# Performance work log

Hardware: AMD Instinct MI355X
Metric: run time of the kernel (lower is better)

The kernel has to match this reference:

```python
import jax, jax.numpy as jnp
import numpy as np

T, B, D, H = 1024, 64, 256, 256


def setup_inputs() -> dict:
    key = jax.random.key(0)
    ks = jax.random.split(key, 7)
    u = lambda k, shape: jax.random.uniform(k, shape, jnp.float32, -0.1, 0.1)
    x = jax.random.normal(ks[0], (T, B, D), dtype=jnp.float32)
    # gate order along last axis: f, g, i, o (each block of width H)
    fwd_W = u(ks[1], (D, 4 * H))
    fwd_U = u(ks[2], (H, 4 * H))
    fwd_b = u(ks[3], (4 * H,))
    bwd_W = u(ks[4], (D, 4 * H))
    bwd_U = u(ks[5], (H, 4 * H))
    bwd_b = u(ks[6], (4 * H,))
    return {"x": x, "fwd_W": fwd_W, "fwd_U": fwd_U, "fwd_b": fwd_b,
            "bwd_W": bwd_W, "bwd_U": bwd_U, "bwd_b": bwd_b}


def _lstm_scan(x, W, U, b):
    # x: [T, B, D]; returns (hs [T,B,H], h_last [B,H])
    Bsz = x.shape[1]
    h0 = jnp.zeros((Bsz, H), x.dtype)
    c0 = jnp.zeros((Bsz, H), x.dtype)
    xW = x @ W  # precompute input projections: [T, B, 4H]

    def step(carry, xw_t):
        h, c = carry
        z = xw_t + h @ U + b  # [B, 4H]
        f = jax.nn.sigmoid(z[:, 0 * H:1 * H])
        g = jnp.tanh(z[:, 1 * H:2 * H])
        i = jax.nn.sigmoid(z[:, 2 * H:3 * H])
        o = jax.nn.sigmoid(z[:, 3 * H:4 * H])
        c_new = c * f + g * i
        h_new = o * jnp.tanh(c_new)
        return (h_new, c_new), h_new

    (h_last, _), hs = jax.lax.scan(step, (h0, c0), xW)
    return hs, h_last


def reference(x, fwd_W, fwd_U, fwd_b, bwd_W, bwd_U, bwd_b):
    hs_f, h_f = _lstm_scan(x, fwd_W, fwd_U, fwd_b)
    hs_b_rev, h_b = _lstm_scan(x[::-1], bwd_W, bwd_U, bwd_b)
    hs_b = hs_b_rev[::-1]
    output = jnp.concatenate([hs_f, hs_b], axis=-1)  # [T, B, 2H]
    return (output, h_f, h_b)
```

## Files before the change

### kernel.cpp

```cpp
#include <hip/hip_runtime.h>

#define T_STEPS 1024
#define BATCH   64
#define NDIM    256
#define HID     256
#define G4      1024

typedef short bf16x8 __attribute__((ext_vector_type(8)));
typedef float f32x4  __attribute__((ext_vector_type(4)));
typedef unsigned short u16;

#define XW_ELEMS ((size_t)2 * T_STEPS * BATCH * G4)
#define UT_ELEMS ((size_t)2 * 4 * 65536)
#define WT_ELEMS UT_ELEMS

__device__ __forceinline__ float b2f(u16 v) {
  union { unsigned u; float f; } c; c.u = ((unsigned)v) << 16; return c.f;
}
__device__ __forceinline__ u16 f2b(float f) {
  union { float f; unsigned u; } c; c.f = f;
  unsigned u = c.u;
  u += 0x7fffu + ((u >> 16) & 1u);
  return (u16)(u >> 16);
}
__device__ __forceinline__ float sigm(float x) {
  float e = __expf(-x);
  return __builtin_amdgcn_rcpf(1.0f + e);
}
__device__ __forceinline__ float tanh_f(float x) {
  return 2.0f * sigm(2.0f * x) - 1.0f;
}

__global__ __launch_bounds__(1024) void build_ut(
    const float* __restrict__ U0, const float* __restrict__ U1,
    u16* __restrict__ UT)
{
  const int d = blockIdx.x >> 2;
  const int g = blockIdx.x & 3;
  const float* __restrict__ U = d ? U1 : U0;
  const int w = threadIdx.x >> 6, lane = threadIdx.x & 63;
  const int q = lane >> 4, c15 = lane & 15;
  u16* dst = UT + ((size_t)d * 4 + g) * 65536;
  #pragma unroll
  for (int kf = 0; kf < 8; ++kf) {
    bf16x8 v;
    #pragma unroll
    for (int j = 0; j < 8; ++j)
      v[j] = (short)f2b(U[(size_t)(kf * 32 + q * 8 + j) * G4 + g * 256 + w * 16 + c15]);
    ((bf16x8*)dst)[((w * 8 + kf) << 6) + lane] = v;
  }
}

__global__ __launch_bounds__(256, 2) void xw_gemm_v2(
    const float* __restrict__ x,
    const u16* __restrict__ WT,
    const float* __restrict__ b0, const float* __restrict__ b1,
    u16* __restrict__ xw)
{
  const int t0   = blockIdx.x * 2;
  const int lane = threadIdx.x & 63;
  const int wv   = threadIdx.x >> 6;
  const int q    = lane >> 4;
  const int c15  = lane & 15;

  __shared__ __align__(16) u16 Alds[2 * 64 * 256];

  #pragma unroll
  for (int t01 = 0; t01 < 2; ++t01) {
    const float* xt = x + (size_t)(t0 + t01) * BATCH * NDIM;
    #pragma unroll
    for (int i = 0; i < 8; ++i) {
      int g = (int)threadIdx.x + 256 * i;
      int r = g >> 5, c = g & 31;
      const float* src = xt + r * 256 + c * 8;
      bf16x8 v;
      #pragma unroll
      for (int j = 0; j < 8; ++j) v[j] = (short)f2b(src[j]);
      int cs = (c & 16) | ((c ^ (r & 15)) & 15);
      ((bf16x8*)Alds)[t01 * 2048 + r * 32 + cs] = v;
    }
  }
  __syncthreads();

  bf16x8 af2[2][8];
  const int arow = wv * 16 + c15;
  #pragma unroll
  for (int t01 = 0; t01 < 2; ++t01) {
    #pragma unroll
    for (int kf = 0; kf < 8; ++kf) {
      int c = kf * 4 + q;
      int cs = (c & 16) | ((c ^ c15) & 15);
      af2[t01][kf] = ((const bf16x8*)Alds)[t01 * 2048 + arow * 32 + cs];
    }
  }

  for (int iter = 0; iter < 32; ++iter) {
    const int d  = iter >> 4;
    const int n0 = (iter & 15) * 64;
    const float* __restrict__ bias = d ? b1 : b0;

    bf16x8 uf[4][8];
    float bc[4];
    #pragma unroll
    for (int ct = 0; ct < 4; ++ct) {
      const int ncol = n0 + ct * 16;
      const int g2 = ncol >> 8, wcol = (ncol >> 4) & 15;
      const bf16x8* wsrc = (const bf16x8*)(WT + ((size_t)d * 4 + g2) * 65536);
      #pragma unroll
      for (int kf = 0; kf < 8; ++kf)
        uf[ct][kf] = wsrc[((wcol * 8 + kf) << 6) + lane];
      bc[ct] = bias[ncol + c15];
    }

    #pragma unroll
    for (int t01 = 0; t01 < 2; ++t01) {
      f32x4 acc[4];
      #pragma unroll
      for (int ct = 0; ct < 4; ++ct) acc[ct] = (f32x4){0.f, 0.f, 0.f, 0.f};
      #pragma unroll
      for (int kf = 0; kf < 8; ++kf) {
        #pragma unroll
        for (int ct = 0; ct < 4; ++ct)
          acc[ct] = __builtin_amdgcn_mfma_f32_16x16x32_bf16(af2[t01][kf], uf[ct][kf], acc[ct], 0, 0, 0);
      }

      u16* dst = xw + (((size_t)d * T_STEPS + (t0 + t01)) * 4 + wv) * 16384;
      #pragma unroll
      for (int ct = 0; ct < 4; ++ct) {
        int ncol = n0 + ct * 16;
        int g2 = ncol >> 8, w2 = (ncol >> 4) & 15;
        union { u16 s[4]; uint2 v; } pk;
        #pragma unroll
        for (int r = 0; r < 4; ++r) pk.s[r] = f2b(acc[ct][r] + bc[ct]);
        *(uint2*)(dst + (size_t)(w2 * 64 + q * 16 + c15) * 16 + g2 * 4) = pk.v;
      }
    }
  }
}

__global__ __launch_bounds__(256, 2) void xw_gemm(
    const float* __restrict__ x,
    const float* __restrict__ W0, const float* __restrict__ W1,
    const float* __restrict__ b0, const float* __restrict__ b1,
    u16* __restrict__ xw)
{
  const int d  = blockIdx.y >> 4;
  const int n0 = (blockIdx.y & 15) * 64;
  const int t0 = blockIdx.x * 32;
  const float* __restrict__ W    = d ? W1 : W0;
  const float* __restrict__ bias = d ? b1 : b0;
  const int lane = threadIdx.x & 63;
  const int wv   = threadIdx.x >> 6;
  const int q    = lane >> 4;
  const int c15  = lane & 15;

  bf16x8 uf[4][8];
  #pragma unroll
  for (int ct = 0; ct < 4; ++ct) {
    const int col = n0 + ct * 16 + c15;
    #pragma unroll
    for (int kf = 0; kf < 8; ++kf) {
      #pragma unroll
      for (int j = 0; j < 8; ++j)
        uf[ct][kf][j] = (short)f2b(W[(size_t)(kf * 32 + q * 8 + j) * G4 + col]);
    }
  }
  float bc[4];
  #pragma unroll
  for (int ct = 0; ct < 4; ++ct) bc[ct] = bias[n0 + ct * 16 + c15];

  __shared__ __align__(16) u16 Alds[64 * 256];

  for (int t = t0; t < t0 + 32; ++t) {
    __syncthreads();
    const float* xt = x + (size_t)t * BATCH * NDIM;
    #pragma unroll
    for (int i = 0; i < 8; ++i) {
      int g = (int)threadIdx.x + 256 * i;
      int r = g >> 5, c = g & 31;
      const float* src = xt + r * 256 + c * 8;
      bf16x8 v;
      #pragma unroll
      for (int j = 0; j < 8; ++j) v[j] = (short)f2b(src[j]);
      int cs = (c & 16) | ((c ^ (r & 15)) & 15);
      ((bf16x8*)Alds)[r * 32 + cs] = v;
    }
    __syncthreads();

    bf16x8 af[8];
    const int arow = wv * 16 + c15;
    #pragma unroll
    for (int kf = 0; kf < 8; ++kf) {
      int c = kf * 4 + q;
      int cs = (c & 16) | ((c ^ c15) & 15);
      af[kf] = ((const bf16x8*)Alds)[arow * 32 + cs];
    }

    f32x4 acc[4];
    #pragma unroll
    for (int ct = 0; ct < 4; ++ct) acc[ct] = (f32x4){0.f, 0.f, 0.f, 0.f};
    #pragma unroll
    for (int kf = 0; kf < 8; ++kf) {
      #pragma unroll
      for (int ct = 0; ct < 4; ++ct)
        acc[ct] = __builtin_amdgcn_mfma_f32_16x16x32_bf16(af[kf], uf[ct][kf], acc[ct], 0, 0, 0);
    }

    u16* dst = xw + (((size_t)d * T_STEPS + t) * 4 + wv) * 16384;
    #pragma unroll
    for (int ct = 0; ct < 4; ++ct) {
      int ncol = n0 + ct * 16;
      int g2 = ncol >> 8, w2 = (ncol >> 4) & 15;
      union { u16 s[4]; uint2 v; } pk;
      #pragma unroll
      for (int r = 0; r < 4; ++r) pk.s[r] = f2b(acc[ct][r] + bc[ct]);
      *(uint2*)(dst + (size_t)(w2 * 64 + q * 16 + c15) * 16 + g2 * 4) = pk.v;
    }
  }
}

__global__ __launch_bounds__(1024) void lstm_scan_fast(
    const u16* __restrict__ xw, const u16* __restrict__ UT,
    float* __restrict__ out)
{
  extern __shared__ __align__(16) u16 dynlds[];
  const int d  = blockIdx.x >> 2;
  const int bt = blockIdx.x & 3;
  const int tid  = threadIdx.x;
  const int w    = tid >> 6;
  const int lane = tid & 63;
  const int q    = lane >> 4;
  const int c15  = lane & 15;

  const u16* __restrict__ UTd = UT + (size_t)d * 4 * 65536;

  bf16x8 uf0[8], uf1[8];
  const bf16x8* UTf = (const bf16x8*)UTd;
  #pragma unroll
  for (int kf = 0; kf < 8; ++kf) {
    uf0[kf] = UTf[       ((w * 8 + kf) << 6) + lane];
    uf1[kf] = UTf[8192 + ((w * 8 + kf) << 6) + lane];
  }

  {
    const int4* src = (const int4*)(UTd + 2 * 65536);
    int4* dstl = (int4*)(dynlds + 8192);
    for (int i = tid; i < 8192; i += 1024) dstl[i] = src[i];
    for (int i = tid; i < 8192; i += 1024) dynlds[i] = 0;
  }

  const int4* __restrict__ Uo4 = (const int4*)(UTd + 3 * 65536);
  const int obase = (w << 9) | lane;
  const char* uib_base = (const char*)(dynlds + 8192) + (size_t)obase * 16;

  int afo[8];
  #pragma unroll
  for (int kf = 0; kf < 8; ++kf) {
    int cc = kf * 4 + q;
    int cs = (cc & 16) | ((cc ^ c15) & 15);
    afo[kf] = (c15 * 32 + cs) * 16;
  }
  const int colv = w * 16 + c15;
  int hwo[4];
  #pragma unroll
  for (int r = 0; r < 4; ++r) {
    int row = q * 4 + r;
    int cch = colv >> 3;
    int cs = (cch & 16) | ((cch ^ row) & 15);
    hwo[r] = ((row * 32 + cs) * 8 + (colv & 7)) * 2;
  }

  float cst[4] = {0.f, 0.f, 0.f, 0.f};
  __syncthreads();

  const int rowbase = bt * 16;
  const size_t hlast_base = (size_t)T_STEPS * BATCH * (2 * HID) + (size_t)d * BATCH * HID;
  const int t_first = d ? (T_STEPS - 1) : 0;

  const long xw_stride = d ? -(long)(4 * 16384) : (long)(4 * 16384);
  const u16* xwp = xw + (((size_t)d * T_STEPS + t_first) * 4 + bt) * 16384 + (size_t)tid * 16;
  union I4x2 { int4 v[2]; u16 s[16]; };
  I4x2 xn;
  xn.v[0] = ((const int4*)xwp)[0];
  xn.v[1] = ((const int4*)xwp)[1];
  xwp += xw_stride;

  int4 ofr[3];
  ofr[0] = Uo4[obase];
  ofr[1] = Uo4[obase + 64];

  float* outp = out + (size_t)(t_first * BATCH + rowbase + q * 4) * (2 * HID)
              + (size_t)d * HID + colv;
  const long out_stride = d ? -(long)(BATCH * 2 * HID) : (long)(BATCH * 2 * HID);

  int curoff = 0;
  for (int it = 0; it < T_STEPS; ++it) {
    f32x4 acc0 = { b2f(xn.s[0]),  b2f(xn.s[1]),  b2f(xn.s[2]),  b2f(xn.s[3])  };
    f32x4 acc1 = { b2f(xn.s[4]),  b2f(xn.s[5]),  b2f(xn.s[6]),  b2f(xn.s[7])  };
    f32x4 acc2 = { b2f(xn.s[8]),  b2f(xn.s[9]),  b2f(xn.s[10]), b2f(xn.s[11]) };
    f32x4 acc3 = { b2f(xn.s[12]), b2f(xn.s[13]), b2f(xn.s[14]), b2f(xn.s[15]) };

    if (it + 1 < T_STEPS) {
      xn.v[0] = ((const int4*)xwp)[0];
      xn.v[1] = ((const int4*)xwp)[1];
      xwp += xw_stride;
    }

    const char* hcb = (const char*)dynlds + curoff;
    bf16x8 afb[2], uib[2];
    afb[0] = *(const bf16x8*)(hcb + afo[0]);
    uib[0] = *(const bf16x8*)(uib_base);
    #pragma unroll
    for (int kf = 0; kf < 8; ++kf) {
      if (kf < 7) {
        afb[(kf + 1) & 1] = *(const bf16x8*)(hcb + afo[kf + 1]);
        uib[(kf + 1) & 1] = *(const bf16x8*)(uib_base + (kf + 1) * 1024);
      }
      if (kf < 6) ofr[(kf + 2) % 3] = Uo4[obase + ((kf + 2) << 6)];
      bf16x8 af = afb[kf & 1];
      union { int4 v; bf16x8 b; } oc; oc.v = ofr[kf % 3];
      acc0 = __builtin_amdgcn_mfma_f32_16x16x32_bf16(af, uf0[kf],     acc0, 0, 0, 0);
      acc1 = __builtin_amdgcn_mfma_f32_16x16x32_bf16(af, uf1[kf],     acc1, 0, 0, 0);
      acc2 = __builtin_amdgcn_mfma_f32_16x16x32_bf16(af, uib[kf & 1], acc2, 0, 0, 0);
      acc3 = __builtin_amdgcn_mfma_f32_16x16x32_bf16(af, oc.b,        acc3, 0, 0, 0);
    }
    ofr[0] = Uo4[obase];
    ofr[1] = Uo4[obase + 64];

    u16 hb[4]; float hv[4];
    #pragma unroll
    for (int r = 0; r < 4; ++r) {
      float fg = sigm(acc0[r]);
      float gg = tanh_f(acc1[r]);
      float ig = sigm(acc2[r]);
      float og = sigm(acc3[r]);
      float cn = cst[r] * fg + gg * ig;
      cst[r] = cn;
      hv[r] = og * tanh_f(cn);
      hb[r] = f2b(hv[r]);
    }

    const int nxtoff = curoff ^ 8192;
    char* hwp = (char*)dynlds + nxtoff;
    #pragma unroll
    for (int r = 0; r < 4; ++r) {
      *(u16*)(hwp + hwo[r]) = hb[r];
      outp[r * (2 * HID)] = hv[r];
    }
    outp += out_stride;
    if (it == T_STEPS - 1) {
      #pragma unroll
      for (int r = 0; r < 4; ++r)
        out[hlast_base + (size_t)(rowbase + q * 4 + r) * HID + colv] = hv[r];
    }
    curoff = nxtoff;
    __syncthreads();
  }
}

__global__ __launch_bounds__(1024) void lstm_scan_safe(
    const u16* __restrict__ xw,
    const float* __restrict__ U0, const float* __restrict__ U1,
    float* __restrict__ out)
{
  const int d  = blockIdx.x >> 2;
  const int bt = blockIdx.x & 3;
  const int tid  = threadIdx.x;
  const int w    = tid >> 6;
  const int lane = tid & 63;
  const int q    = lane >> 4;
  const int c15  = lane & 15;
  const float* __restrict__ U = d ? U1 : U0;

  bf16x8 uf[4][8];
  #pragma unroll
  for (int g = 0; g < 4; ++g) {
    const int col2 = g * 256 + w * 16 + c15;
    #pragma unroll
    for (int kf = 0; kf < 8; ++kf) {
      #pragma unroll
      for (int j = 0; j < 8; ++j)
        uf[g][kf][j] = (short)f2b(U[(size_t)(kf * 32 + q * 8 + j) * G4 + col2]);
    }
  }

  __shared__ __align__(16) u16 hbuf[2][16 * 256];
  for (int i = tid; i < 16 * 256; i += 1024) { hbuf[0][i] = 0; hbuf[1][i] = 0; }
  float cst[4] = {0.f, 0.f, 0.f, 0.f};
  __syncthreads();

  const int rowbase = bt * 16;
  const int col = w * 16 + c15;
  const size_t hlast_base = (size_t)T_STEPS * BATCH * (2 * HID) + (size_t)d * BATCH * HID;

  for (int it = 0; it < T_STEPS; ++it) {
    const int t = d ? (T_STEPS - 1 - it) : it;
    union { int4 v[2]; u16 s[16]; } xv;
    {
      const int4* xwt = (const int4*)(xw + ((((size_t)d * T_STEPS + t) * 4 + bt) * 1024 + tid) * 16);
      xv.v[0] = xwt[0]; xv.v[1] = xwt[1];
    }
    const int cur = it & 1;
    bf16x8 af[8];
    #pragma unroll
    for (int kf = 0; kf < 8; ++kf) {
      int cc = kf * 4 + q;
      int cs = (cc & 16) | ((cc ^ c15) & 15);
      af[kf] = ((const bf16x8*)hbuf[cur])[c15 * 32 + cs];
    }
    f32x4 acc[4];
    #pragma unroll
    for (int g = 0; g < 4; ++g) acc[g] = (f32x4){0.f, 0.f, 0.f, 0.f};
    #pragma unroll
    for (int kf = 0; kf < 8; ++kf)
      #pragma unroll
      for (int g = 0; g < 4; ++g)
        acc[g] = __builtin_amdgcn_mfma_f32_16x16x32_bf16(af[kf], uf[g][kf], acc[g], 0, 0, 0);

    u16 hb[4]; float hv[4];
    #pragma unroll
    for (int r = 0; r < 4; ++r) {
      float zf = acc[0][r] + b2f(xv.s[0 * 4 + r]);
      float zg = acc[1][r] + b2f(xv.s[1 * 4 + r]);
      float zi = acc[2][r] + b2f(xv.s[2 * 4 + r]);
      float zo = acc[3][r] + b2f(xv.s[3 * 4 + r]);
      float fg = sigm(zf), gg = tanh_f(zg), ig = sigm(zi), og = sigm(zo);
      float cn = cst[r] * fg + gg * ig;
      cst[r] = cn;
      hv[r] = og * tanh_f(cn);
      hb[r] = f2b(hv[r]);
    }
    const int nxt = cur ^ 1;
    #pragma unroll
    for (int r = 0; r < 4; ++r) {
      const int row = q * 4 + r;
      int cch = col >> 3;
      int cs = (cch & 16) | ((cch ^ row) & 15);
      hbuf[nxt][(row * 32 + cs) * 8 + (col & 7)] = hb[r];
      out[((size_t)t * BATCH + rowbase + row) * (2 * HID) + (size_t)d * HID + col] = hv[r];
    }
    if (it == T_STEPS - 1) {
      #pragma unroll
      for (int r = 0; r < 4; ++r)
        out[hlast_base + (size_t)(rowbase + q * 4 + r) * HID + col] = hv[r];
    }
    __syncthreads();
  }
}

extern "C" void kernel_launch(void* const* d_in, const int* in_sizes, int n_in,
                              void* d_out, int out_size, void* d_ws, size_t ws_size,
                              hipStream_t stream) {
  const float* x  = (const float*)d_in[0];
  const float* fW = (const float*)d_in[1];
  const float* fU = (const float*)d_in[2];
  const float* fb = (const float*)d_in[3];
  const float* bW = (const float*)d_in[4];
  const float* bU = (const float*)d_in[5];
  const float* bb = (const float*)d_in[6];
  u16*   xwbuf = (u16*)d_ws;
  u16*   UT    = (u16*)d_ws + XW_ELEMS;
  u16*   WT    = (u16*)d_ws + XW_ELEMS + UT_ELEMS;
  float* out   = (float*)d_out;

  const bool fast   = ws_size >= (XW_ELEMS + UT_ELEMS) * sizeof(u16);
  const bool use_v2 = ws_size >= (XW_ELEMS + UT_ELEMS + WT_ELEMS) * sizeof(u16);

  if (use_v2) {
    build_ut<<<8, 1024, 0, stream>>>(fW, bW, WT);
    xw_gemm_v2<<<512, 256, 0, stream>>>(x, WT, fb, bb, xwbuf);
  } else {
    dim3 g1(32, 32);
    xw_gemm<<<g1, 256, 0, stream>>>(x, fW, bW, fb, bb, xwbuf);
  }
  if (fast) {
    build_ut<<<8, 1024, 0, stream>>>(fU, bU, UT);
    hipFuncSetAttribute((const void*)lstm_scan_fast,
                        hipFuncAttributeMaxDynamicSharedMemorySize, 147456);
    lstm_scan_fast<<<8, 1024, 147456, stream>>>(xwbuf, UT, out);
  } else {
    lstm_scan_safe<<<8, 1024, 0, stream>>>(xwbuf, fU, bU, out);
  }
}
```

Measured before the change: 3.977 ms.

## Pre-convert x to bf16 MFMA fragments and restructure input-projection GEMM grid

Adds a kernel that converts x to bf16 once and stores it in MFMA fragment order. The input-projection GEMM is replaced by a 2D-grid version in which each block keeps its W column tile in registers, converting from fp32 on load, and streams 32 timesteps of pre-packed A fragments with double-buffered prefetch. This removes the old version's repeated per-block x conversion and the W transpose pre-pass, at the cost of an extra bf16 buffer round trip through memory. The recurrent scan, which likely dominates total time, is unchanged.

```diff
diff --git a/kernel.cpp b/kernel.cpp
--- a/kernel.cpp
+++ b/kernel.cpp
@@ -10,9 +10,9 @@
 typedef float f32x4  __attribute__((ext_vector_type(4)));
 typedef unsigned short u16;
 
-#define XW_ELEMS ((size_t)2 * T_STEPS * BATCH * G4)
-#define UT_ELEMS ((size_t)2 * 4 * 65536)
-#define WT_ELEMS UT_ELEMS
+#define XW_ELEMS  ((size_t)2 * T_STEPS * BATCH * G4)
+#define UT_ELEMS  ((size_t)2 * 4 * 65536)
+#define XBF_ELEMS ((size_t)T_STEPS * BATCH * NDIM)
 
 __device__ __forceinline__ float b2f(u16 v) {
   union { unsigned u; float f; } c; c.u = ((unsigned)v) << 16; return c.f;
@@ -51,69 +51,83 @@
   }
 }
 
-__global__ __launch_bounds__(256, 2) void xw_gemm_v2(
-    const float* __restrict__ x,
-    const u16* __restrict__ WT,
+__global__ __launch_bounds__(256) void x_to_frag(
+    const float* __restrict__ x, u16* __restrict__ xbf)
+{
+  const int t   = blockIdx.x;
+  const int tid = threadIdx.x;
+  const int wv  = tid >> 6, lane = tid & 63;
+  const int q   = lane >> 4, c15 = lane & 15;
+  __shared__ __align__(16) u16 Alds[64 * 256];
+
+  const float* xt = x + (size_t)t * BATCH * NDIM;
+  #pragma unroll
+  for (int i = 0; i < 8; ++i) {
+    int g = tid + 256 * i;
+    int r = g >> 5, c = g & 31;
+    const float* src = xt + r * 256 + c * 8;
+    bf16x8 v;
+    #pragma unroll
+    for (int j = 0; j < 8; ++j) v[j] = (short)f2b(src[j]);
+    int cs = (c & 16) | ((c ^ (r & 15)) & 15);
+    ((bf16x8*)Alds)[r * 32 + cs] = v;
+  }
+  __syncthreads();
+
+  const int arow = wv * 16 + c15;
+  #pragma unroll
+  for (int kf = 0; kf < 8; ++kf) {
+    int c = kf * 4 + q;
+    int cs = (c & 16) | ((c ^ c15) & 15);
+    bf16x8 v = ((const bf16x8*)Alds)[arow * 32 + cs];
+    ((bf16x8*)xbf)[(((size_t)t * 4 + wv) * 8 + kf) * 64 + lane] = v;
+  }
+}
+
+__global__ __launch_bounds__(256, 2) void xw_gemm_v3(
+    const u16* __restrict__ xbf,
+    const float* __restrict__ W0, const float* __restrict__ W1,
     const float* __restrict__ b0, const float* __restrict__ b1,
     u16* __restrict__ xw)
 {
-  const int t0   = blockIdx.x * 2;
+  const int d  = blockIdx.y >> 4;
+  const int n0 = (blockIdx.y & 15) * 64;
+  const int t0 = blockIdx.x * 32;
+  const float* __restrict__ W    = d ? W1 : W0;
+  const float* __restrict__ bias = d ? b1 : b0;
   const int lane = threadIdx.x & 63;
   const int wv   = threadIdx.x >> 6;
   const int q    = lane >> 4;
   const int c15  = lane & 15;
 
-  __shared__ __align__(16) u16 Alds[2 * 64 * 256];
-
-  #pragma unroll
-  for (int t01 = 0; t01 < 2; ++t01) {
-    const float* xt = x + (size_t)(t0 + t01) * BATCH * NDIM;
-    #pragma unroll
-    for (int i = 0; i < 8; ++i) {
-      int g = (int)threadIdx.x + 256 * i;
-      int r = g >> 5, c = g & 31;
-      const float* src = xt + r * 256 + c * 8;
-      bf16x8 v;
-      #pragma unroll
-      for (int j = 0; j < 8; ++j) v[j] = (short)f2b(src[j]);
-      int cs = (c & 16) | ((c ^ (r & 15)) & 15);
-      ((bf16x8*)Alds)[t01 * 2048 + r * 32 + cs] = v;
-    }
-  }
-  __syncthreads();
-
-  bf16x8 af2[2][8];
-  const int arow = wv * 16 + c15;
-  #pragma unroll
-  for (int t01 = 0; t01 < 2; ++t01) {
-    #pragma unroll
-    for (int kf = 0; kf < 8; ++kf) {
-      int c = kf * 4 + q;
-      int cs = (c & 16) | ((c ^ c15) & 15);
-      af2[t01][kf] = ((const bf16x8*)Alds)[t01 * 2048 + arow * 32 + cs];
-    }
-  }
-
-  for (int iter = 0; iter < 32; ++iter) {
-    const int d  = iter >> 4;
-    const int n0 = (iter & 15) * 64;
-    const float* __restrict__ bias = d ? b1 : b0;
-
-    bf16x8 uf[4][8];
-    float bc[4];
-    #pragma unroll
-    for (int ct = 0; ct < 4; ++ct) {
-      const int ncol = n0 + ct * 16;
-      const int g2 = ncol >> 8, wcol = (ncol >> 4) & 15;
-      const bf16x8* wsrc = (const bf16x8*)(WT + ((size_t)d * 4 + g2) * 65536);
-      #pragma unroll
-      for (int kf = 0; kf < 8; ++kf)
-        uf[ct][kf] = wsrc[((wcol * 8 + kf) << 6) + lane];
-      bc[ct] = bias[ncol + c15];
-    }
-
-    #pragma unroll
-    for (int t01 = 0; t01 < 2; ++t01) {
+  bf16x8 uf[4][8];
+  #pragma unroll
+  for (int ct = 0; ct < 4; ++ct) {
+    const int col = n0 + ct * 16 + c15;
+    #pragma unroll
+    for (int kf = 0; kf < 8; ++kf) {
+      #pragma unroll
+      for (int j = 0; j < 8; ++j)
+        uf[ct][kf][j] = (short)f2b(W[(size_t)(kf * 32 + q * 8 + j) * G4 + col]);
+    }
+  }
+  float bc[4];
+  #pragma unroll
+  for (int ct = 0; ct < 4; ++ct) bc[ct] = bias[n0 + ct * 16 + c15];
+
+  const bf16x8* __restrict__ xb = (const bf16x8*)xbf;
+  const size_t wvl = (size_t)wv * 8 * 64 + lane;
+  #define AFIDX(t, kf) (((size_t)(t) * 32 + (kf)) * 64 + wvl)
+
+  bf16x8 afA[8], afB[8];
+  #pragma unroll
+  for (int kf = 0; kf < 8; ++kf) afA[kf] = xb[AFIDX(t0, kf)];
+
+  for (int tt = t0; tt < t0 + 32; tt += 2) {
+    #pragma unroll
+    for (int kf = 0; kf < 8; ++kf) afB[kf] = xb[AFIDX(tt + 1, kf)];
+
+    {
       f32x4 acc[4];
       #pragma unroll
       for (int ct = 0; ct < 4; ++ct) acc[ct] = (f32x4){0.f, 0.f, 0.f, 0.f};
@@ -121,10 +135,9 @@
       for (int kf = 0; kf < 8; ++kf) {
         #pragma unroll
         for (int ct = 0; ct < 4; ++ct)
-          acc[ct] = __builtin_amdgcn_mfma_f32_16x16x32_bf16(af2[t01][kf], uf[ct][kf], acc[ct], 0, 0, 0);
+          acc[ct] = __builtin_amdgcn_mfma_f32_16x16x32_bf16(afA[kf], uf[ct][kf], acc[ct], 0, 0, 0);
       }
-
-      u16* dst = xw + (((size_t)d * T_STEPS + (t0 + t01)) * 4 + wv) * 16384;
+      u16* dst = xw + (((size_t)d * T_STEPS + tt) * 4 + wv) * 16384;
       #pragma unroll
       for (int ct = 0; ct < 4; ++ct) {
         int ncol = n0 + ct * 16;
@@ -135,7 +148,35 @@
         *(uint2*)(dst + (size_t)(w2 * 64 + q * 16 + c15) * 16 + g2 * 4) = pk.v;
       }
     }
-  }
+
+    if (tt + 2 < t0 + 32) {
+      #pragma unroll
+      for (int kf = 0; kf < 8; ++kf) afA[kf] = xb[AFIDX(tt + 2, kf)];
+    }
+
+    {
+      f32x4 acc[4];
+      #pragma unroll
+      for (int ct = 0; ct < 4; ++ct) acc[ct] = (f32x4){0.f, 0.f, 0.f, 0.f};
+      #pragma unroll
+      for (int kf = 0; kf < 8; ++kf) {
+        #pragma unroll
+        for (int ct = 0; ct < 4; ++ct)
+          acc[ct] = __builtin_amdgcn_mfma_f32_16x16x32_bf16(afB[kf], uf[ct][kf], acc[ct], 0, 0, 0);
+      }
+      u16* dst = xw + (((size_t)d * T_STEPS + (tt + 1)) * 4 + wv) * 16384;
+      #pragma unroll
+      for (int ct = 0; ct < 4; ++ct) {
+        int ncol = n0 + ct * 16;
+        int g2 = ncol >> 8, w2 = (ncol >> 4) & 15;
+        union { u16 s[4]; uint2 v; } pk;
+        #pragma unroll
+        for (int r = 0; r < 4; ++r) pk.s[r] = f2b(acc[ct][r] + bc[ct]);
+        *(uint2*)(dst + (size_t)(w2 * 64 + q * 16 + c15) * 16 + g2 * 4) = pk.v;
+      }
+    }
+  }
+  #undef AFIDX
 }
 
 __global__ __launch_bounds__(256, 2) void xw_gemm(
@@ -460,15 +501,16 @@
   const float* bb = (const float*)d_in[6];
   u16*   xwbuf = (u16*)d_ws;
   u16*   UT    = (u16*)d_ws + XW_ELEMS;
-  u16*   WT    = (u16*)d_ws + XW_ELEMS + UT_ELEMS;
+  u16*   XBF   = (u16*)d_ws + XW_ELEMS + UT_ELEMS;
   float* out   = (float*)d_out;
 
   const bool fast   = ws_size >= (XW_ELEMS + UT_ELEMS) * sizeof(u16);
-  const bool use_v2 = ws_size >= (XW_ELEMS + UT_ELEMS + WT_ELEMS) * sizeof(u16);
-
-  if (use_v2) {
-    build_ut<<<8, 1024, 0, stream>>>(fW, bW, WT);
-    xw_gemm_v2<<<512, 256, 0, stream>>>(x, WT, fb, bb, xwbuf);
+  const bool use_v3 = ws_size >= (XW_ELEMS + UT_ELEMS + XBF_ELEMS) * sizeof(u16);
+
+  if (use_v3) {
+    x_to_frag<<<1024, 256, 0, stream>>>(x, XBF);
+    dim3 g1(32, 32);
+    xw_gemm_v3<<<g1, 256, 0, stream>>>(XBF, fW, bW, fb, bb, xwbuf);
   } else {
     dim3 g1(32, 32);
     xw_gemm<<<g1, 256, 0, stream>>>(x, fW, bW, fb, bb, xwbuf);
```

New measurement: 3.871 ms. -2.7%, faster.
